# Performance work log

Measured on AMD Instinct MI355X. Metric: run time of the kernel, lower is better.

## Reference

```python
import jax, jax.numpy as jnp
import numpy as np

N = 50000
E = 1600000
IN_CH = 64


def _sage_conv(x, edge_index, W_l, b_l, W_r):
    # PyG SAGEConv with mean aggregation:
    #   out = lin_l(mean_{j in N(i)} x_j) + lin_r(x_i)
    src, dst = edge_index[0], edge_index[1]
    n = x.shape[0]
    msg_sum = jax.ops.segment_sum(x[src], dst, num_segments=n)          # [N, d_in]
    cnt = jax.ops.segment_sum(jnp.ones((src.shape[0],), x.dtype), dst,
                              num_segments=n)                            # [N]
    agg = msg_sum / jnp.maximum(cnt, 1.0)[:, None]                       # mean, 0 if no nbrs
    return agg @ W_l.T + b_l + x @ W_r.T


def setup_inputs() -> dict:
    key = jax.random.key(0)
    ks = jax.random.split(key, 9)
    x = jax.random.normal(ks[0], (N, IN_CH), dtype=jnp.float32)
    edge_index = jax.random.randint(ks[1], (2, E), 0, N, dtype=jnp.int64)
    s = 1.0 / np.sqrt(IN_CH)
    W1_l = jax.random.uniform(ks[2], (64, IN_CH), jnp.float32, -s, s)
    b1_l = jnp.zeros((64,), jnp.float32)
    W1_r = jax.random.uniform(ks[3], (64, IN_CH), jnp.float32, -s, s)
    s2 = 1.0 / np.sqrt(64)
    W2_l = jax.random.uniform(ks[4], (32, 64), jnp.float32, -s2, s2)
    b2_l = jnp.zeros((32,), jnp.float32)
    W2_r = jax.random.uniform(ks[5], (32, 64), jnp.float32, -s2, s2)
    s3 = 1.0 / np.sqrt(32)
    W_lin = jax.random.uniform(ks[6], (1, 32), jnp.float32, -s3, s3)
    b_lin = jax.random.uniform(ks[7], (1,), jnp.float32, -s3, s3)
    return {"x": x, "edge_index": edge_index,
            "W1_l": W1_l, "b1_l": b1_l, "W1_r": W1_r,
            "W2_l": W2_l, "b2_l": b2_l, "W2_r": W2_r,
            "W_lin": W_lin, "b_lin": b_lin}


def reference(x, edge_index, W1_l, b1_l, W1_r, W2_l, b2_l, W2_r, W_lin, b_lin):
    h = jax.nn.relu(_sage_conv(x, edge_index, W1_l, b1_l, W1_r))   # [N, 64]
    h = jax.nn.relu(_sage_conv(h, edge_index, W2_l, b2_l, W2_r))   # [N, 32]
    return h @ W_lin.T + b_lin                                      # [N, 1]
```

## Files before the change

### kernel.cpp

```cpp
#include <hip/hip_runtime.h>
#include <cstdint>
#include <cstddef>

using u8  = unsigned char;
using u16 = unsigned short;
using u32 = unsigned int;

typedef short short8 __attribute__((ext_vector_type(8)));
typedef float f32x4 __attribute__((ext_vector_type(4)));

#define NB 256
#define HCAP4 12544

__device__ __forceinline__ float bf2f(u16 h) { return __uint_as_float(((u32)h) << 16); }
__device__ __forceinline__ u16 f2bf(float f) {
    u32 u = __float_as_uint(f);
    u += 0x7FFFu + ((u >> 16) & 1u);
    return (u16)(u >> 16);
}

__device__ __forceinline__ void load8(const float* p, float* v) {
    float4 a = ((const float4*)p)[0];
    float4 b = ((const float4*)p)[1];
    v[0]=a.x; v[1]=a.y; v[2]=a.z; v[3]=a.w;
    v[4]=b.x; v[5]=b.y; v[6]=b.z; v[7]=b.w;
}
__device__ __forceinline__ void load8(const u16* p, float* v) {
    uint4 u = *(const uint4*)p;
    v[0]=__uint_as_float(u.x << 16); v[1]=__uint_as_float(u.x & 0xFFFF0000u);
    v[2]=__uint_as_float(u.y << 16); v[3]=__uint_as_float(u.y & 0xFFFF0000u);
    v[4]=__uint_as_float(u.z << 16); v[5]=__uint_as_float(u.z & 0xFFFF0000u);
    v[6]=__uint_as_float(u.w << 16); v[7]=__uint_as_float(u.w & 0xFFFF0000u);
}
__device__ __forceinline__ void store8bf(u16* p, const float* v) {
    uint4 w;
    w.x = (u32)f2bf(v[0]) | ((u32)f2bf(v[1]) << 16);
    w.y = (u32)f2bf(v[2]) | ((u32)f2bf(v[3]) << 16);
    w.z = (u32)f2bf(v[4]) | ((u32)f2bf(v[5]) << 16);
    w.w = (u32)f2bf(v[6]) | ((u32)f2bf(v[7]) << 16);
    *(uint4*)p = w;
}
__device__ __forceinline__ short8 ld8b(const u16* p) {
    union { uint4 u; short8 s; } c;
    c.u = *(const uint4*)p;
    return c.s;
}
__device__ __forceinline__ void acc8(const uint4& u, float* a) {
    a[0]+=__uint_as_float(u.x << 16); a[1]+=__uint_as_float(u.x & 0xFFFF0000u);
    a[2]+=__uint_as_float(u.y << 16); a[3]+=__uint_as_float(u.y & 0xFFFF0000u);
    a[4]+=__uint_as_float(u.z << 16); a[5]+=__uint_as_float(u.z & 0xFFFF0000u);
    a[6]+=__uint_as_float(u.w << 16); a[7]+=__uint_as_float(u.w & 0xFFFF0000u);
}

__global__ __launch_bounds__(1024) void hist_lds_kernel(const int* idx,
                                                        const float* __restrict__ x,
                                                        u16* __restrict__ xh,
                                                        u16* __restrict__ xl,
                                                        u32* __restrict__ mat,
                                                        u8* __restrict__ within,
                                                        u32* __restrict__ pe,
                                                        int E, int n, int total8) {
    __shared__ u32 h[HCAP4];
    __shared__ int s_nz;
    const int t = threadIdx.x;
    const int b = blockIdx.x;
    const int hw4 = (n + 3) >> 2;
    if (t == 0) s_nz = 0;
    for (int w = t; w < hw4; w += 1024) h[w] = 0;
    if (t < 128 && ((const u32*)idx)[2 * t + 1] != 0u) atomicOr(&s_nz, 1);

    {
        const int nt = (total8 + NB - 1) / NB;
        const int c1 = min(b * nt + nt, total8);
        for (int c = b * nt + t; c < c1; c += 1024) {
            float v[8], lo[8];
            load8(x + (size_t)c * 8, v);
            #pragma unroll
            for (int k = 0; k < 8; ++k) lo[k] = v[k] - bf2f(f2bf(v[k]));
            store8bf(xh + (size_t)c * 8, v);
            store8bf(xl + (size_t)c * 8, lo);
        }
    }
    __syncthreads();
    const int stride = s_nz ? 1 : 2;
    const int chunk = (E + NB - 1) / NB;
    const int e1 = min(b * chunk + chunk, E);
    for (int e = b * chunk + t; e < e1; e += 1024) {
        const int s = idx[(size_t)e * stride];
        const int d = idx[(size_t)(E + e) * stride];
        const int sh = (d & 3) << 3;
        const u32 old = atomicAdd(&h[d >> 2], 1u << sh);
        within[e] = (u8)((old >> sh) & 0xFFu);
        pe[e] = ((u32)d << 16) | (u32)s;
    }
    __syncthreads();
    u32* dst = mat + (size_t)b * hw4;
    for (int w = t; w < hw4; w += 1024) dst[w] = h[w];
}

__global__ __launch_bounds__(256) void csr_base_kernel(u32* __restrict__ mat,
                                                       int* __restrict__ deg,
                                                       int* __restrict__ bsum64, int n) {
    __shared__ u32 gs[16][17];
    __shared__ int s_bs[16];
    const int hw4 = (n + 3) >> 2;
    const int wl = threadIdx.x & 15;
    const int j  = threadIdx.x >> 4;
    const int w = blockIdx.x * 16 + wl;
    if (threadIdx.x < 16) s_bs[threadIdx.x] = 0;
    u32 c[16];
    u32 s = 0;
    if (w < hw4) {
        #pragma unroll
        for (int k = 0; k < 16; ++k) {
            c[k] = mat[(size_t)(j * 16 + k) * hw4 + w];
            s += c[k];
        }
    }
    gs[j][wl] = s;
    __syncthreads();
    u32 run = 0, total = 0;
    for (int g = 0; g < 16; ++g) {
        const u32 v = gs[g][wl];
        if (g < j) run += v;
        total += v;
    }
    if (w < hw4) {
        #pragma unroll
        for (int k = 0; k < 16; ++k) {
            const size_t o = (size_t)(j * 16 + k) * hw4 + w;
            const u32 v = c[k];
            mat[o] = run;
            run += v;
        }
        if (j == 0) {
            int ds = 0;
            #pragma unroll
            for (int q = 0; q < 4; ++q) {
                const int node = 4 * w + q;
                const int dv = (int)((total >> (q << 3)) & 0xFFu);
                if (node < n) { deg[node] = dv; ds += dv; }
            }
            s_bs[wl] = ds;
        }
    }
    __syncthreads();
    if (threadIdx.x == 0) {
        int bs = 0;
        #pragma unroll
        for (int k = 0; k < 16; ++k) bs += s_bs[k];
        bsum64[blockIdx.x] = bs;
    }
}

__global__ __launch_bounds__(256) void scan_write_kernel(const int* __restrict__ deg,
                                                         const int* __restrict__ bsum64,
                                                         int* __restrict__ row_ptr,
                                                         int n, int nb64) {
    __shared__ int wr[4];
    __shared__ int ws[4];
    __shared__ int s_boff;
    const int t = threadIdx.x;
    const int lane = t & 63, wv = t >> 6;
    const int lim = 4 * blockIdx.x;
    int pv = 0;
    {
        const int k0 = t * 4;
        #pragma unroll
        for (int jj = 0; jj < 4; ++jj) {
            const int k = k0 + jj;
            if (k < lim && k < nb64) pv += bsum64[k];
        }
    }
    #pragma unroll
    for (int o = 1; o < 64; o <<= 1) pv += __shfl_xor(pv, o, 64);
    if (lane == 0) wr[wv] = pv;
    __syncthreads();
    if (t == 0) s_boff = wr[0] + wr[1] + wr[2] + wr[3];
    const int i = blockIdx.x * 256 + t;
    const int x = (i < n) ? deg[i] : 0;
    int v = x;
    #pragma unroll
    for (int o = 1; o < 64; o <<= 1) {
        int u = __shfl_up(v, o, 64);
        if (lane >= o) v += u;
    }
    if (lane == 63) ws[wv] = v;
    __syncthreads();
    int woff = s_boff;
    for (int w = 0; w < wv; ++w) woff += ws[w];
    const int excl = v - x + woff;
    if (i < n) row_ptr[i] = excl;
    if (i == n - 1) row_ptr[n] = excl + x;
}

__global__ __launch_bounds__(1024) void scatter_kernel(const u32* __restrict__ pe,
                                                       const u32* __restrict__ mat,
                                                       const int* __restrict__ row_ptr,
                                                       const u8* __restrict__ within,
                                                       u16* __restrict__ ssrc, int E, int n) {
    const int hw4 = (n + 3) >> 2;
    const int chunk = (E + NB - 1) / NB;
    const int b = blockIdx.x;
    const int e1 = min(b * chunk + chunk, E);
    const u32* base = mat + (size_t)b * hw4;
    for (int e = b * chunk + threadIdx.x; e < e1; e += 1024) {
        const u32 p = pe[e];
        const int s = (int)(p & 0xFFFFu);
        const int d = (int)(p >> 16);
        const int wb = (int)((base[d >> 2] >> ((d & 3) << 3)) & 0xFFu);
        ssrc[row_ptr[d] + wb + (int)within[e]] = (u16)s;
    }
}

__global__ __launch_bounds__(256) void agg64_kernel(const u16* __restrict__ feat,
                                                    const int* __restrict__ row_ptr,
                                                    const u16* __restrict__ ssrc,
                                                    u16* __restrict__ out, int n) {
    const int lane = threadIdx.x & 63;
    const int wid = (blockIdx.x * blockDim.x + threadIdx.x) >> 6;
    const int nw = (gridDim.x * blockDim.x) >> 6;
    const int g = lane >> 3;
    const int q = lane & 7;
    for (int i = wid; i < n; i += nw) {
        const int rb = row_ptr[i], re = row_ptr[i + 1];
        float acc0[8], acc1[8];
        #pragma unroll
        for (int k = 0; k < 8; ++k) { acc0[k] = 0.f; acc1[k] = 0.f; }
        int e = rb + g;
        for (; e + 24 < re; e += 32) {
            const int s0 = (int)ssrc[e];
            const int s1 = (int)ssrc[e + 8];
            const int s2 = (int)ssrc[e + 16];
            const int s3 = (int)ssrc[e + 24];
            const uint4 u0 = *(const uint4*)(feat + (size_t)s0 * 64 + q * 8);
            const uint4 u1 = *(const uint4*)(feat + (size_t)s1 * 64 + q * 8);
            const uint4 u2 = *(const uint4*)(feat + (size_t)s2 * 64 + q * 8);
            const uint4 u3 = *(const uint4*)(feat + (size_t)s3 * 64 + q * 8);
            acc8(u0, acc0); acc8(u1, acc1); acc8(u2, acc0); acc8(u3, acc1);
        }
        for (; e + 8 < re; e += 16) {
            const int s0 = (int)ssrc[e];
            const int s1 = (int)ssrc[e + 8];
            const uint4 u0 = *(const uint4*)(feat + (size_t)s0 * 64 + q * 8);
            const uint4 u1 = *(const uint4*)(feat + (size_t)s1 * 64 + q * 8);
            acc8(u0, acc0); acc8(u1, acc1);
        }
        if (e < re) {
            const int s0 = (int)ssrc[e];
            const uint4 u0 = *(const uint4*)(feat + (size_t)s0 * 64 + q * 8);
            acc8(u0, acc0);
        }
        #pragma unroll
        for (int k = 0; k < 8; ++k) acc0[k] += acc1[k];
        #pragma unroll
        for (int m = 8; m < 64; m <<= 1) {
            #pragma unroll
            for (int k = 0; k < 8; ++k) acc0[k] += __shfl_xor(acc0[k], m, 64);
        }
        if (g == 0) {
            float inv = 1.0f / (float)max(re - rb, 1);
            #pragma unroll
            for (int k = 0; k < 8; ++k) acc0[k] *= inv;
            store8bf(out + (size_t)i * 64 + q * 8, acc0);
        }
    }
}

#define W1P 140
#define W2P 76
__global__ __launch_bounds__(256) void layer1_mfma_kernel(
    const u16* __restrict__ A1b, const u16* __restrict__ xh, const u16* __restrict__ xl,
    const float* __restrict__ W1l, const float* __restrict__ b1,
    const float* __restrict__ W1r, const float* __restrict__ W2l,
    const float* __restrict__ b2, const float* __restrict__ W2r,
    u16* __restrict__ z2, float* __restrict__ r2, int n)
{
    __shared__ alignas(16) u16 w1h[64 * W1P], w1l[64 * W1P];
    __shared__ alignas(16) u16 w2h[64 * W2P], w2l[64 * W2P];
    __shared__ alignas(16) u16 h1h[64 * W2P], h1l[64 * W2P];

    const int t = threadIdx.x;
    for (int c = t; c < 64 * 32; c += 256) {
        const int ch = c >> 5, k = (c & 31) * 4;
        const float* src = (k < 64) ? (W1l + ch * 64 + k) : (W1r + ch * 64 + (k - 64));
        float4 w = *(const float4*)src;
        const float wv[4] = {w.x, w.y, w.z, w.w};
        #pragma unroll
        for (int j = 0; j < 4; ++j) {
            u16 h = f2bf(wv[j]);
            w1h[ch * W1P + k + j] = h;
            w1l[ch * W1P + k + j] = f2bf(wv[j] - bf2f(h));
        }
    }
    for (int c = t; c < 64 * 16; c += 256) {
        const int ch = c >> 4, k = (c & 15) * 4;
        const float* src = (ch < 32) ? (W2l + ch * 64 + k) : (W2r + (ch - 32) * 64 + k);
        float4 w = *(const float4*)src;
        const float wv[4] = {w.x, w.y, w.z, w.w};
        #pragma unroll
        for (int j = 0; j < 4; ++j) {
            u16 h = f2bf(wv[j]);
            w2h[ch * W2P + k + j] = h;
            w2l[ch * W2P + k + j] = f2bf(wv[j] - bf2f(h));
        }
    }
    __syncthreads();

    const int lane = t & 63;
    const int wv = t >> 6;
    const int m = lane & 15, quad = lane >> 4;
    const int base = blockIdx.x * 64 + wv * 16;

    const int nodeA = min(base + m, n - 1);
    const u16* a1row = A1b + (size_t)nodeA * 64;
    const u16* xhrow = xh + (size_t)nodeA * 64;
    const u16* xlrow = xl + (size_t)nodeA * 64;
    short8 aA[2], aH[2], aL[2];
    aA[0] = ld8b(a1row + quad * 8);      aA[1] = ld8b(a1row + 32 + quad * 8);
    aH[0] = ld8b(xhrow + quad * 8);      aH[1] = ld8b(xhrow + 32 + quad * 8);
    aL[0] = ld8b(xlrow + quad * 8);      aL[1] = ld8b(xlrow + 32 + quad * 8);

    #pragma unroll
    for (int ni = 0; ni < 4; ++ni) {
        const int row = ni * 16 + m;
        f32x4 acc = {0.f, 0.f, 0.f, 0.f};
        #pragma unroll
        for (int kc = 0; kc < 2; ++kc) {
            short8 b = ld8b(&w1h[row * W1P + kc * 32 + quad * 8]);
            acc = __builtin_amdgcn_mfma_f32_16x16x32_bf16(aA[kc], b, acc, 0, 0, 0);
        }
        #pragma unroll
        for (int kc = 0; kc < 2; ++kc) {
            short8 bh = ld8b(&w1h[row * W1P + 64 + kc * 32 + quad * 8]);
            short8 bl = ld8b(&w1l[row * W1P + 64 + kc * 32 + quad * 8]);
            acc = __builtin_amdgcn_mfma_f32_16x16x32_bf16(aH[kc], bh, acc, 0, 0, 0);
            acc = __builtin_amdgcn_mfma_f32_16x16x32_bf16(aH[kc], bl, acc, 0, 0, 0);
            acc = __builtin_amdgcn_mfma_f32_16x16x32_bf16(aL[kc], bh, acc, 0, 0, 0);
        }
        const float bias = b1[row];
        #pragma unroll
        for (int r = 0; r < 4; ++r) {
            float h = fmaxf(acc[r] + bias, 0.0f);
            u16 hh = f2bf(h);
            h1h[(wv * 16 + quad * 4 + r) * W2P + row] = hh;
            h1l[(wv * 16 + quad * 4 + r) * W2P + row] = f2bf(h - bf2f(hh));
        }
    }

    short8 ah[2], al[2];
    ah[0] = ld8b(&h1h[(wv * 16 + m) * W2P + quad * 8]);
    ah[1] = ld8b(&h1h[(wv * 16 + m) * W2P + 32 + quad * 8]);
    al[0] = ld8b(&h1l[(wv * 16 + m) * W2P + quad * 8]);
    al[1] = ld8b(&h1l[(wv * 16 + m) * W2P + 32 + quad * 8]);

    #pragma unroll
    for (int ni = 0; ni < 4; ++ni) {
        const int row = ni * 16 + m;
        f32x4 acc = {0.f, 0.f, 0.f, 0.f};
        #pragma unroll
        for (int kc = 0; kc < 2; ++kc) {
            short8 bh = ld8b(&w2h[row * W2P + kc * 32 + quad * 8]);
            short8 bl = ld8b(&w2l[row * W2P + kc * 32 + quad * 8]);
            acc = __builtin_amdgcn_mfma_f32_16x16x32_bf16(ah[kc], bh, acc, 0, 0, 0);
            acc = __builtin_amdgcn_mfma_f32_16x16x32_bf16(ah[kc], bl, acc, 0, 0, 0);
            acc = __builtin_amdgcn_mfma_f32_16x16x32_bf16(al[kc], bh, acc, 0, 0, 0);
        }
        if (ni < 2) {
            #pragma unroll
            for (int r = 0; r < 4; ++r) {
                int node = base + quad * 4 + r;
                if (node < n) z2[(size_t)node * 32 + row] = f2bf(acc[r]);
            }
        } else {
            const int ch = row - 32;
            const float bias = b2[ch];
            #pragma unroll
            for (int r = 0; r < 4; ++r) {
                int node = base + quad * 4 + r;
                if (node < n) r2[(size_t)node * 32 + ch] = acc[r] + bias;
            }
        }
    }
}

__global__ __launch_bounds__(256) void layer2_final_kernel(
    const u16* __restrict__ z2, const float* __restrict__ r2,
    const int* __restrict__ row_ptr, const u16* __restrict__ ssrc,
    const float* __restrict__ Wlin, const float* __restrict__ blin,
    float* __restrict__ out, int n)
{
    const int lane = threadIdx.x & 63;
    const int wid = (blockIdx.x * blockDim.x + threadIdx.x) >> 6;
    const int nw = (gridDim.x * blockDim.x) >> 6;
    const int g = lane >> 2;
    const int q = lane & 3;
    float wlin8[8];
    load8(Wlin + q * 8, wlin8);
    const float bl = blin[0];
    for (int i = wid; i < n; i += nw) {
        const int rb = row_ptr[i], re = row_ptr[i + 1];
        float acc0[8], acc1[8];
        #pragma unroll
        for (int k = 0; k < 8; ++k) { acc0[k] = 0.f; acc1[k] = 0.f; }
        int e = rb + g;
        for (; e + 16 < re; e += 32) {
            const int s0 = (int)ssrc[e];
            const int s1 = (int)ssrc[e + 16];
            const uint4 u0 = *(const uint4*)(z2 + (size_t)s0 * 32 + q * 8);
            const uint4 u1 = *(const uint4*)(z2 + (size_t)s1 * 32 + q * 8);
            acc8(u0, acc0); acc8(u1, acc1);
        }
        if (e < re) {
            const int s0 = (int)ssrc[e];
            const uint4 u0 = *(const uint4*)(z2 + (size_t)s0 * 32 + q * 8);
            acc8(u0, acc0);
        }
        #pragma unroll
        for (int k = 0; k < 8; ++k) acc0[k] += acc1[k];
        #pragma unroll
        for (int m = 4; m < 64; m <<= 1) {
            #pragma unroll
            for (int k = 0; k < 8; ++k) acc0[k] += __shfl_xor(acc0[k], m, 64);
        }
        float partial = 0.0f;
        if (g == 0) {
            const float inv = 1.0f / (float)max(re - rb, 1);
            float r2v[8];
            load8(r2 + (size_t)i * 32 + q * 8, r2v);
            #pragma unroll
            for (int k = 0; k < 8; ++k)
                partial += fmaxf(fmaf(acc0[k], inv, r2v[k]), 0.0f) * wlin8[k];
        }
        partial += __shfl_xor(partial, 1, 64);
        partial += __shfl_xor(partial, 2, 64);
        if (lane == 0) out[i] = partial + bl;
    }
}

extern "C" void kernel_launch(void* const* d_in, const int* in_sizes, int n_in,
                              void* d_out, int out_size, void* d_ws, size_t ws_size,
                              hipStream_t stream) {
    (void)n_in; (void)out_size; (void)ws_size;
    const int N = in_sizes[0] / 64;
    const int E = in_sizes[1] / 2;
    const int hw4 = (N + 3) >> 2;
    const int nb64 = (hw4 + 15) / 16;

    char* ws = (char*)d_ws;
    size_t off = 0;
    auto alloc = [&](size_t bytes) -> void* {
        void* p = ws + off;
        off += (bytes + 255) & ~(size_t)255;
        return p;
    };
    u32*   mat     = (u32*)alloc((size_t)NB * hw4 * 4);
    u8*    within  = (u8*)alloc((size_t)E);
    u32*   pe      = (u32*)alloc((size_t)E * 4);
    int*   deg     = (int*)alloc((size_t)N * 4);
    int*   row_ptr = (int*)alloc(((size_t)N + 1) * 4);
    u16*   ssrc    = (u16*)alloc((size_t)E * 2);
    int*   bsum64  = (int*)alloc((size_t)nb64 * 4);
    u16*   xh      = (u16*)alloc((size_t)N * 64 * 2);
    u16*   xl      = (u16*)alloc((size_t)N * 64 * 2);
    u16*   A1b     = (u16*)alloc((size_t)N * 64 * 2);
    u16*   z2      = (u16*)alloc((size_t)N * 32 * 2);
    float* r2      = (float*)alloc((size_t)N * 32 * 4);

    const int* idx = (const int*)d_in[1];
    const int nb2 = (N + 255) / 256;

    hist_lds_kernel<<<NB, 1024, 0, stream>>>(idx, (const float*)d_in[0], xh, xl,
                                             mat, within, pe, E, N, N * 8);
    csr_base_kernel<<<(hw4 + 15) / 16, 256, 0, stream>>>(mat, deg, bsum64, N);
    scan_write_kernel<<<nb2, 256, 0, stream>>>(deg, bsum64, row_ptr, N, nb64);
    scatter_kernel<<<NB, 1024, 0, stream>>>(pe, mat, row_ptr, within, ssrc, E, N);

    agg64_kernel<<<2048, 256, 0, stream>>>(xh, row_ptr, ssrc, A1b, N);

    layer1_mfma_kernel<<<(N + 63) / 64, 256, 0, stream>>>(A1b, xh, xl,
        (const float*)d_in[2], (const float*)d_in[3], (const float*)d_in[4],
        (const float*)d_in[5], (const float*)d_in[6], (const float*)d_in[7],
        z2, r2, N);

    layer2_final_kernel<<<2048, 256, 0, stream>>>(z2, r2, row_ptr, ssrc,
        (const float*)d_in[8], (const float*)d_in[9], (float*)d_out, N);
}
```

Before: 222.1 us.

## Replace per-block LDS histogram CSR build with global atomic counting sort

Drops the 256-block LDS histogram, the per-block offset matrix and its transposed prefix scan. In their place it counts degrees with global atomics, runs a single-block scan to get row pointers, and scatters sources using atomic cursors. This removes the large mat buffer traffic (256 x N/4 words written and read twice) and two kernel launches. In exchange it adds global atomic contention, a serial single-workgroup scan, and a nondeterministic edge order within each row, which can change float summation order.

Measured after the change: 486.6 us. +119.1%, slower.

```diff
diff --git a/kernel.cpp b/kernel.cpp
--- a/kernel.cpp
+++ b/kernel.cpp
@@ -9,8 +9,6 @@
 typedef short short8 __attribute__((ext_vector_type(8)));
 typedef float f32x4 __attribute__((ext_vector_type(4)));
 
-#define NB 256
-#define HCAP4 12544
 
 __device__ __forceinline__ float bf2f(u16 h) { return __uint_as_float(((u32)h) << 16); }
 __device__ __forceinline__ u16 f2bf(float f) {
@@ -52,164 +50,84 @@
     a[6]+=__uint_as_float(u.w << 16); a[7]+=__uint_as_float(u.w & 0xFFFF0000u);
 }
 
-__global__ __launch_bounds__(1024) void hist_lds_kernel(const int* idx,
+__global__ __launch_bounds__(256) void deg_split_kernel(const int* idx,
                                                         const float* __restrict__ x,
                                                         u16* __restrict__ xh,
                                                         u16* __restrict__ xl,
-                                                        u32* __restrict__ mat,
-                                                        u8* __restrict__ within,
                                                         u32* __restrict__ pe,
-                                                        int E, int n, int total8) {
-    __shared__ u32 h[HCAP4];
+                                                        int* __restrict__ deg,
+                                                        int E, int total8) {
     __shared__ int s_nz;
     const int t = threadIdx.x;
-    const int b = blockIdx.x;
-    const int hw4 = (n + 3) >> 2;
+    const int gid = blockIdx.x * 256 + t;
+    const int gsz = gridDim.x * 256;
     if (t == 0) s_nz = 0;
-    for (int w = t; w < hw4; w += 1024) h[w] = 0;
+    __syncthreads();
     if (t < 128 && ((const u32*)idx)[2 * t + 1] != 0u) atomicOr(&s_nz, 1);
 
-    {
-        const int nt = (total8 + NB - 1) / NB;
-        const int c1 = min(b * nt + nt, total8);
-        for (int c = b * nt + t; c < c1; c += 1024) {
-            float v[8], lo[8];
-            load8(x + (size_t)c * 8, v);
-            #pragma unroll
-            for (int k = 0; k < 8; ++k) lo[k] = v[k] - bf2f(f2bf(v[k]));
-            store8bf(xh + (size_t)c * 8, v);
-            store8bf(xl + (size_t)c * 8, lo);
-        }
+    for (int c = gid; c < total8; c += gsz) {
+        float v[8], lo[8];
+        load8(x + (size_t)c * 8, v);
+        #pragma unroll
+        for (int k = 0; k < 8; ++k) lo[k] = v[k] - bf2f(f2bf(v[k]));
+        store8bf(xh + (size_t)c * 8, v);
+        store8bf(xl + (size_t)c * 8, lo);
     }
     __syncthreads();
     const int stride = s_nz ? 1 : 2;
-    const int chunk = (E + NB - 1) / NB;
-    const int e1 = min(b * chunk + chunk, E);
-    for (int e = b * chunk + t; e < e1; e += 1024) {
+    for (int e = gid; e < E; e += gsz) {
         const int s = idx[(size_t)e * stride];
         const int d = idx[(size_t)(E + e) * stride];
-        const int sh = (d & 3) << 3;
-        const u32 old = atomicAdd(&h[d >> 2], 1u << sh);
-        within[e] = (u8)((old >> sh) & 0xFFu);
         pe[e] = ((u32)d << 16) | (u32)s;
-    }
-    __syncthreads();
-    u32* dst = mat + (size_t)b * hw4;
-    for (int w = t; w < hw4; w += 1024) dst[w] = h[w];
-}
-
-__global__ __launch_bounds__(256) void csr_base_kernel(u32* __restrict__ mat,
-                                                       int* __restrict__ deg,
-                                                       int* __restrict__ bsum64, int n) {
-    __shared__ u32 gs[16][17];
-    __shared__ int s_bs[16];
-    const int hw4 = (n + 3) >> 2;
-    const int wl = threadIdx.x & 15;
-    const int j  = threadIdx.x >> 4;
-    const int w = blockIdx.x * 16 + wl;
-    if (threadIdx.x < 16) s_bs[threadIdx.x] = 0;
-    u32 c[16];
-    u32 s = 0;
-    if (w < hw4) {
-        #pragma unroll
-        for (int k = 0; k < 16; ++k) {
-            c[k] = mat[(size_t)(j * 16 + k) * hw4 + w];
-            s += c[k];
-        }
-    }
-    gs[j][wl] = s;
-    __syncthreads();
-    u32 run = 0, total = 0;
-    for (int g = 0; g < 16; ++g) {
-        const u32 v = gs[g][wl];
-        if (g < j) run += v;
-        total += v;
-    }
-    if (w < hw4) {
-        #pragma unroll
-        for (int k = 0; k < 16; ++k) {
-            const size_t o = (size_t)(j * 16 + k) * hw4 + w;
-            const u32 v = c[k];
-            mat[o] = run;
-            run += v;
-        }
-        if (j == 0) {
-            int ds = 0;
-            #pragma unroll
-            for (int q = 0; q < 4; ++q) {
-                const int node = 4 * w + q;
-                const int dv = (int)((total >> (q << 3)) & 0xFFu);
-                if (node < n) { deg[node] = dv; ds += dv; }
-            }
-            s_bs[wl] = ds;
-        }
-    }
-    __syncthreads();
-    if (threadIdx.x == 0) {
-        int bs = 0;
-        #pragma unroll
-        for (int k = 0; k < 16; ++k) bs += s_bs[k];
-        bsum64[blockIdx.x] = bs;
-    }
-}
-
-__global__ __launch_bounds__(256) void scan_write_kernel(const int* __restrict__ deg,
-                                                         const int* __restrict__ bsum64,
-                                                         int* __restrict__ row_ptr,
-                                                         int n, int nb64) {
-    __shared__ int wr[4];
-    __shared__ int ws[4];
-    __shared__ int s_boff;
+        atomicAdd(&deg[d], 1);
+    }
+}
+
+__global__ __launch_bounds__(1024) void scan_kernel(const int* __restrict__ deg,
+                                                    int* __restrict__ row_ptr,
+                                                    int* __restrict__ cur, int n) {
+    __shared__ int wsum[16];
     const int t = threadIdx.x;
+    const int per = (n + 1023) >> 10;
+    const int b0 = t * per;
+    int s = 0;
+    for (int j = 0; j < per; ++j) {
+        const int i = b0 + j;
+        if (i < n) s += deg[i];
+    }
     const int lane = t & 63, wv = t >> 6;
-    const int lim = 4 * blockIdx.x;
-    int pv = 0;
-    {
-        const int k0 = t * 4;
-        #pragma unroll
-        for (int jj = 0; jj < 4; ++jj) {
-            const int k = k0 + jj;
-            if (k < lim && k < nb64) pv += bsum64[k];
-        }
-    }
-    #pragma unroll
-    for (int o = 1; o < 64; o <<= 1) pv += __shfl_xor(pv, o, 64);
-    if (lane == 0) wr[wv] = pv;
-    __syncthreads();
-    if (t == 0) s_boff = wr[0] + wr[1] + wr[2] + wr[3];
-    const int i = blockIdx.x * 256 + t;
-    const int x = (i < n) ? deg[i] : 0;
-    int v = x;
+    int v = s;
     #pragma unroll
     for (int o = 1; o < 64; o <<= 1) {
         int u = __shfl_up(v, o, 64);
         if (lane >= o) v += u;
     }
-    if (lane == 63) ws[wv] = v;
+    if (lane == 63) wsum[wv] = v;
     __syncthreads();
-    int woff = s_boff;
-    for (int w = 0; w < wv; ++w) woff += ws[w];
-    const int excl = v - x + woff;
-    if (i < n) row_ptr[i] = excl;
-    if (i == n - 1) row_ptr[n] = excl + x;
-}
-
-__global__ __launch_bounds__(1024) void scatter_kernel(const u32* __restrict__ pe,
-                                                       const u32* __restrict__ mat,
-                                                       const int* __restrict__ row_ptr,
-                                                       const u8* __restrict__ within,
-                                                       u16* __restrict__ ssrc, int E, int n) {
-    const int hw4 = (n + 3) >> 2;
-    const int chunk = (E + NB - 1) / NB;
-    const int b = blockIdx.x;
-    const int e1 = min(b * chunk + chunk, E);
-    const u32* base = mat + (size_t)b * hw4;
-    for (int e = b * chunk + threadIdx.x; e < e1; e += 1024) {
+    int woff = 0;
+    for (int w = 0; w < wv; ++w) woff += wsum[w];
+    int run = v - s + woff;
+    for (int j = 0; j < per; ++j) {
+        const int i = b0 + j;
+        if (i < n) {
+            row_ptr[i] = run;
+            cur[i] = run;
+            run += deg[i];
+        }
+    }
+    if (t == 1023) row_ptr[n] = run;
+}
+
+__global__ __launch_bounds__(256) void scatter_atomic_kernel(const u32* __restrict__ pe,
+                                                             int* __restrict__ cur,
+                                                             u16* __restrict__ ssrc, int E) {
+    const int gid = blockIdx.x * 256 + threadIdx.x;
+    const int gsz = gridDim.x * 256;
+    for (int e = gid; e < E; e += gsz) {
         const u32 p = pe[e];
-        const int s = (int)(p & 0xFFFFu);
         const int d = (int)(p >> 16);
-        const int wb = (int)((base[d >> 2] >> ((d & 3) << 3)) & 0xFFu);
-        ssrc[row_ptr[d] + wb + (int)within[e]] = (u16)s;
+        const int pos = atomicAdd(&cur[d], 1);
+        ssrc[pos] = (u16)(p & 0xFFFFu);
     }
 }
 
@@ -444,8 +362,6 @@
     (void)n_in; (void)out_size; (void)ws_size;
     const int N = in_sizes[0] / 64;
     const int E = in_sizes[1] / 2;
-    const int hw4 = (N + 3) >> 2;
-    const int nb64 = (hw4 + 15) / 16;
 
     char* ws = (char*)d_ws;
     size_t off = 0;
@@ -454,13 +370,11 @@
         off += (bytes + 255) & ~(size_t)255;
         return p;
     };
-    u32*   mat     = (u32*)alloc((size_t)NB * hw4 * 4);
-    u8*    within  = (u8*)alloc((size_t)E);
     u32*   pe      = (u32*)alloc((size_t)E * 4);
     int*   deg     = (int*)alloc((size_t)N * 4);
+    int*   cur     = (int*)alloc((size_t)N * 4);
     int*   row_ptr = (int*)alloc(((size_t)N + 1) * 4);
     u16*   ssrc    = (u16*)alloc((size_t)E * 2);
-    int*   bsum64  = (int*)alloc((size_t)nb64 * 4);
     u16*   xh      = (u16*)alloc((size_t)N * 64 * 2);
     u16*   xl      = (u16*)alloc((size_t)N * 64 * 2);
     u16*   A1b     = (u16*)alloc((size_t)N * 64 * 2);
@@ -468,13 +382,13 @@
     float* r2      = (float*)alloc((size_t)N * 32 * 4);
 
     const int* idx = (const int*)d_in[1];
-    const int nb2 = (N + 255) / 256;
-
-    hist_lds_kernel<<<NB, 1024, 0, stream>>>(idx, (const float*)d_in[0], xh, xl,
-                                             mat, within, pe, E, N, N * 8);
-    csr_base_kernel<<<(hw4 + 15) / 16, 256, 0, stream>>>(mat, deg, bsum64, N);
-    scan_write_kernel<<<nb2, 256, 0, stream>>>(deg, bsum64, row_ptr, N, nb64);
-    scatter_kernel<<<NB, 1024, 0, stream>>>(pe, mat, row_ptr, within, ssrc, E, N);
+
+    hipMemsetAsync(deg, 0, (size_t)N * 4, stream);
+
+    deg_split_kernel<<<2048, 256, 0, stream>>>(idx, (const float*)d_in[0], xh, xl,
+                                               pe, deg, E, N * 8);
+    scan_kernel<<<1, 1024, 0, stream>>>(deg, row_ptr, cur, N);
+    scatter_atomic_kernel<<<2048, 256, 0, stream>>>(pe, cur, ssrc, E);
 
     agg64_kernel<<<2048, 256, 0, stream>>>(xh, row_ptr, ssrc, A1b, N);
 
```

## Split layer-1 aggregation into two half-width passes and drop bf16 low-part buffer

Applied to the files above, without the earlier changes.

Layer-1 neighbour aggregation now runs as two launches, each gathering 32 of the 64 channels (64 bytes per row). This shrinks the working set of each pass so the gathered half of the feature table fits better in cache. The separate xl low-part buffer is removed, and layer1 now reads fp32 x directly and splits it into bf16 hi/lo in registers, which saves a write and a read of a full bf16 array. The cost is an extra kernel launch, reading the edge list twice, and more shuffle reduction steps per node.

After: 242.9 us. 1.09x slower.

```diff
diff --git a/kernel.cpp b/kernel.cpp
--- a/kernel.cpp
+++ b/kernel.cpp
@@ -55,7 +55,6 @@
 __global__ __launch_bounds__(1024) void hist_lds_kernel(const int* idx,
                                                         const float* __restrict__ x,
                                                         u16* __restrict__ xh,
-                                                        u16* __restrict__ xl,
                                                         u32* __restrict__ mat,
                                                         u8* __restrict__ within,
                                                         u32* __restrict__ pe,
@@ -73,12 +72,9 @@
         const int nt = (total8 + NB - 1) / NB;
         const int c1 = min(b * nt + nt, total8);
         for (int c = b * nt + t; c < c1; c += 1024) {
-            float v[8], lo[8];
+            float v[8];
             load8(x + (size_t)c * 8, v);
-            #pragma unroll
-            for (int k = 0; k < 8; ++k) lo[k] = v[k] - bf2f(f2bf(v[k]));
             store8bf(xh + (size_t)c * 8, v);
-            store8bf(xl + (size_t)c * 8, lo);
         }
     }
     __syncthreads();
@@ -213,48 +209,37 @@
     }
 }
 
-__global__ __launch_bounds__(256) void agg64_kernel(const u16* __restrict__ feat,
+__global__ __launch_bounds__(256) void agg32_kernel(const u16* __restrict__ feat,
                                                     const int* __restrict__ row_ptr,
                                                     const u16* __restrict__ ssrc,
-                                                    u16* __restrict__ out, int n) {
+                                                    u16* __restrict__ out, int n, int coff) {
     const int lane = threadIdx.x & 63;
     const int wid = (blockIdx.x * blockDim.x + threadIdx.x) >> 6;
     const int nw = (gridDim.x * blockDim.x) >> 6;
-    const int g = lane >> 3;
-    const int q = lane & 7;
+    const int g = lane >> 2;
+    const int q = lane & 3;
     for (int i = wid; i < n; i += nw) {
         const int rb = row_ptr[i], re = row_ptr[i + 1];
         float acc0[8], acc1[8];
         #pragma unroll
         for (int k = 0; k < 8; ++k) { acc0[k] = 0.f; acc1[k] = 0.f; }
         int e = rb + g;
-        for (; e + 24 < re; e += 32) {
+        for (; e + 16 < re; e += 32) {
             const int s0 = (int)ssrc[e];
-            const int s1 = (int)ssrc[e + 8];
-            const int s2 = (int)ssrc[e + 16];
-            const int s3 = (int)ssrc[e + 24];
-            const uint4 u0 = *(const uint4*)(feat + (size_t)s0 * 64 + q * 8);
-            const uint4 u1 = *(const uint4*)(feat + (size_t)s1 * 64 + q * 8);
-            const uint4 u2 = *(const uint4*)(feat + (size_t)s2 * 64 + q * 8);
-            const uint4 u3 = *(const uint4*)(feat + (size_t)s3 * 64 + q * 8);
-            acc8(u0, acc0); acc8(u1, acc1); acc8(u2, acc0); acc8(u3, acc1);
-        }
-        for (; e + 8 < re; e += 16) {
-            const int s0 = (int)ssrc[e];
-            const int s1 = (int)ssrc[e + 8];
-            const uint4 u0 = *(const uint4*)(feat + (size_t)s0 * 64 + q * 8);
-            const uint4 u1 = *(const uint4*)(feat + (size_t)s1 * 64 + q * 8);
+            const int s1 = (int)ssrc[e + 16];
+            const uint4 u0 = *(const uint4*)(feat + (size_t)s0 * 64 + coff + q * 8);
+            const uint4 u1 = *(const uint4*)(feat + (size_t)s1 * 64 + coff + q * 8);
             acc8(u0, acc0); acc8(u1, acc1);
         }
         if (e < re) {
             const int s0 = (int)ssrc[e];
-            const uint4 u0 = *(const uint4*)(feat + (size_t)s0 * 64 + q * 8);
+            const uint4 u0 = *(const uint4*)(feat + (size_t)s0 * 64 + coff + q * 8);
             acc8(u0, acc0);
         }
         #pragma unroll
         for (int k = 0; k < 8; ++k) acc0[k] += acc1[k];
         #pragma unroll
-        for (int m = 8; m < 64; m <<= 1) {
+        for (int m = 4; m < 64; m <<= 1) {
             #pragma unroll
             for (int k = 0; k < 8; ++k) acc0[k] += __shfl_xor(acc0[k], m, 64);
         }
@@ -262,7 +247,7 @@
             float inv = 1.0f / (float)max(re - rb, 1);
             #pragma unroll
             for (int k = 0; k < 8; ++k) acc0[k] *= inv;
-            store8bf(out + (size_t)i * 64 + q * 8, acc0);
+            store8bf(out + (size_t)i * 64 + coff + q * 8, acc0);
         }
     }
 }
@@ -270,7 +255,7 @@
 #define W1P 140
 #define W2P 76
 __global__ __launch_bounds__(256) void layer1_mfma_kernel(
-    const u16* __restrict__ A1b, const u16* __restrict__ xh, const u16* __restrict__ xl,
+    const u16* __restrict__ A1b, const float* __restrict__ x,
     const float* __restrict__ W1l, const float* __restrict__ b1,
     const float* __restrict__ W1r, const float* __restrict__ W2l,
     const float* __restrict__ b2, const float* __restrict__ W2r,
@@ -314,12 +299,23 @@
 
     const int nodeA = min(base + m, n - 1);
     const u16* a1row = A1b + (size_t)nodeA * 64;
-    const u16* xhrow = xh + (size_t)nodeA * 64;
-    const u16* xlrow = xl + (size_t)nodeA * 64;
+    const float* xrow = x + (size_t)nodeA * 64;
     short8 aA[2], aH[2], aL[2];
     aA[0] = ld8b(a1row + quad * 8);      aA[1] = ld8b(a1row + 32 + quad * 8);
-    aH[0] = ld8b(xhrow + quad * 8);      aH[1] = ld8b(xhrow + 32 + quad * 8);
-    aL[0] = ld8b(xlrow + quad * 8);      aL[1] = ld8b(xlrow + 32 + quad * 8);
+    {
+        float v0[8], v1[8];
+        load8(xrow + quad * 8, v0);
+        load8(xrow + 32 + quad * 8, v1);
+        union { u16 h[8]; short8 s; } H0, L0, H1, L1;
+        #pragma unroll
+        for (int k = 0; k < 8; ++k) {
+            u16 hh = f2bf(v0[k]);
+            H0.h[k] = hh; L0.h[k] = f2bf(v0[k] - bf2f(hh));
+            u16 hh1 = f2bf(v1[k]);
+            H1.h[k] = hh1; L1.h[k] = f2bf(v1[k] - bf2f(hh1));
+        }
+        aH[0] = H0.s; aL[0] = L0.s; aH[1] = H1.s; aL[1] = L1.s;
+    }
 
     #pragma unroll
     for (int ni = 0; ni < 4; ++ni) {
@@ -462,7 +458,6 @@
     u16*   ssrc    = (u16*)alloc((size_t)E * 2);
     int*   bsum64  = (int*)alloc((size_t)nb64 * 4);
     u16*   xh      = (u16*)alloc((size_t)N * 64 * 2);
-    u16*   xl      = (u16*)alloc((size_t)N * 64 * 2);
     u16*   A1b     = (u16*)alloc((size_t)N * 64 * 2);
     u16*   z2      = (u16*)alloc((size_t)N * 32 * 2);
     float* r2      = (float*)alloc((size_t)N * 32 * 4);
@@ -470,15 +465,16 @@
     const int* idx = (const int*)d_in[1];
     const int nb2 = (N + 255) / 256;
 
-    hist_lds_kernel<<<NB, 1024, 0, stream>>>(idx, (const float*)d_in[0], xh, xl,
+    hist_lds_kernel<<<NB, 1024, 0, stream>>>(idx, (const float*)d_in[0], xh,
                                              mat, within, pe, E, N, N * 8);
     csr_base_kernel<<<(hw4 + 15) / 16, 256, 0, stream>>>(mat, deg, bsum64, N);
     scan_write_kernel<<<nb2, 256, 0, stream>>>(deg, bsum64, row_ptr, N, nb64);
     scatter_kernel<<<NB, 1024, 0, stream>>>(pe, mat, row_ptr, within, ssrc, E, N);
 
-    agg64_kernel<<<2048, 256, 0, stream>>>(xh, row_ptr, ssrc, A1b, N);
-
-    layer1_mfma_kernel<<<(N + 63) / 64, 256, 0, stream>>>(A1b, xh, xl,
+    agg32_kernel<<<2048, 256, 0, stream>>>(xh, row_ptr, ssrc, A1b, N, 0);
+    agg32_kernel<<<2048, 256, 0, stream>>>(xh, row_ptr, ssrc, A1b, N, 32);
+
+    layer1_mfma_kernel<<<(N + 63) / 64, 256, 0, stream>>>(A1b, (const float*)d_in[0],
         (const float*)d_in[2], (const float*)d_in[3], (const float*)d_in[4],
         (const float*)d_in[5], (const float*)d_in[6], (const float*)d_in[7],
         z2, r2, N);
```
